# Performance work log

Measured on AMD Instinct MI355X. Metric: run time of the kernel, lower is better.

The kernel has to match this reference:

```python
import jax, jax.numpy as jnp
from jax import lax
import numpy as np

PROB = 0.4
SNR_LO, SNR_HI = 0.5, 3.0
BF_LO, BF_HI = 0.1, 0.5
MAX_CH = 0.5
FS = 256
B, C, T = 64, 64, 15360


def setup_inputs() -> dict:
    key = jax.random.key(0)
    ks = jax.random.split(key, 8)
    return {
        "x": jax.random.normal(ks[0], (B, C, T), dtype=jnp.float32),
        "noise": jax.random.normal(ks[1], (B, C, T), dtype=jnp.float32),
        "apply_u": jax.random.uniform(ks[2], (B,), dtype=jnp.float32),
        "frac_u": jax.random.uniform(ks[3], (B,), dtype=jnp.float32),
        "ch_u": jax.random.uniform(ks[4], (B, C), dtype=jnp.float32),
        "burst_u": jax.random.uniform(ks[5], (B,), dtype=jnp.float32),
        "start_u": jax.random.uniform(ks[6], (B,), dtype=jnp.float32),
        "snr_u": jax.random.uniform(ks[7], (B,), dtype=jnp.float32),
    }


def _emg_inject(x, noise, apply_u, frac_u, ch_u, burst_u, start_u, snr_u):
    b, c, t = x.shape
    # --- highpass: noise - moving average (torch conv1d, zero pad) ---
    k = max(3, FS // 10)
    if k % 2 == 0:
        k += 1  # -> 25
    ker = jnp.ones((1, 1, k), noise.dtype) / k
    low = lax.conv_general_dilated(
        noise.reshape(b * c, 1, t), ker, (1,), [(k // 2, k // 2)],
        dimension_numbers=("NCH", "OIH", "NCH")).reshape(b, c, t)
    emg = noise - low  # (B,C,T)

    # --- per-sample burst mask with linear edge ramps ---
    blen = lax.stop_gradient(jnp.floor(t * (BF_LO + burst_u * (BF_HI - BF_LO))).astype(jnp.int32))  # (B,)
    start = lax.stop_gradient(jnp.floor(start_u * jnp.maximum(t - blen, 1).astype(jnp.float32)).astype(jnp.int32))
    elen = jnp.minimum(25, blen // 4)

    tt = jnp.arange(t, dtype=jnp.float32)[None, :]          # (1,T)
    sf = start.astype(jnp.float32)[:, None]                  # (B,1)
    bf = blen.astype(jnp.float32)[:, None]
    ef = elen.astype(jnp.float32)[:, None]
    end = sf + bf
    denom = jnp.maximum(ef - 1.0, 1.0)
    in_burst = (tt >= sf) & (tt < end)
    up = (tt - sf) / denom                                   # linspace(0,1,elen)
    down = (end - 1.0 - tt) / denom                          # linspace(1,0,elen)
    ramped = jnp.where(tt < sf + ef, up, jnp.where(tt >= end - ef, down, 1.0))
    mask = jnp.where(in_burst, jnp.where(ef > 1.0, ramped, 1.0), 0.0)  # (B,T)

    # --- random affected-channel subset (randperm[:n_affected]) ---
    n_aff = jnp.maximum(1, jnp.floor(c * frac_u * MAX_CH).astype(jnp.int32))  # (B,)
    ch_rank = jnp.argsort(jnp.argsort(ch_u, axis=1), axis=1)                  # (B,C)
    ch_mask = (ch_rank < n_aff[:, None]).astype(x.dtype)                      # (B,C)

    emg_b = emg * mask[:, None, :]
    sig_p = jnp.sqrt(jnp.mean(x * x, axis=-1, keepdims=True)) + 1e-8          # (B,C,1)
    noi_p = jnp.sqrt(jnp.mean(emg_b * emg_b, axis=-1, keepdims=True)) + 1e-8
    snr = (SNR_LO + snr_u * (SNR_HI - SNR_LO))[:, None, None]
    scaled = emg_b * (sig_p / (noi_p * snr))

    sel = (apply_u <= PROB).astype(x.dtype)[:, None, None] * ch_mask[:, :, None]
    return x + sel * scaled


def reference(x, noise, apply_u, frac_u, ch_u, burst_u, start_u, snr_u):
    return _emg_inject(x, noise, apply_u, frac_u, ch_u, burst_u, start_u, snr_u)
```

## Files before the change

### kernel.cpp

```cpp
#include <hip/hip_runtime.h>
#include <math.h>

constexpr int T_LEN = 15360;
constexpr int B_DIM = 64;
constexpr int C_DIM = 64;
constexpr int NTHR  = 256;
constexpr int PT    = T_LEN / NTHR;
constexpr int VPT   = T_LEN / 4 / NTHR;
constexpr int KHALF = 12;

__global__ __launch_bounds__(NTHR, 2)
void emg_inject_kernel(const float* __restrict__ x,
                       const float* __restrict__ noise,
                       const float* __restrict__ apply_u,
                       const float* __restrict__ frac_u,
                       const float* __restrict__ ch_u,
                       const float* __restrict__ burst_u,
                       const float* __restrict__ start_u,
                       const float* __restrict__ snr_u,
                       float* __restrict__ out)
{
    const int row = blockIdx.x;
    const int b   = row >> 6;
    const int c   = row & 63;
    const int tid = threadIdx.x;

    __shared__ float s_ch[C_DIM];
    __shared__ float s_red[8];
    __shared__ float s_noise[T_LEN];

    if (tid < C_DIM) s_ch[tid] = ch_u[(size_t)b * C_DIM + tid];
    __syncthreads();

    const float myv = s_ch[c];
    int rank = 0;
    #pragma unroll 8
    for (int i = 0; i < C_DIM; ++i) {
        float v = s_ch[i];
        rank += (v < myv || (v == myv && i < c)) ? 1 : 0;
    }
    const float frac = frac_u[b];
    int n_aff = (int)floorf(((float)C_DIM * frac) * 0.5f);
    n_aff = max(1, n_aff);
    const bool affected = (apply_u[b] <= 0.4f) && (rank < n_aff);

    const float*  xrow = x   + (size_t)row * T_LEN;
    float*        orow = out + (size_t)row * T_LEN;
    const float4* x4   = (const float4*)xrow;
    float4*       o4   = (float4*)orow;

    if (!affected) {
        #pragma unroll
        for (int it = 0; it < VPT; ++it) {
            int idx = tid + it * NTHR;
            o4[idx] = x4[idx];
        }
        return;
    }

    const float4* n4 = (const float4*)(noise + (size_t)row * T_LEN);
    float4* s_n4 = (float4*)s_noise;
    float4 xr[VPT];
    float sumx2 = 0.f;
    #pragma unroll
    for (int it = 0; it < VPT; ++it) {
        int idx = tid + it * NTHR;
        float4 nv = n4[idx];
        s_n4[idx] = nv;
        float4 xv = x4[idx];
        xr[it] = xv;
        sumx2 += xv.x * xv.x + xv.y * xv.y + xv.z * xv.z + xv.w * xv.w;
    }

    const float bu   = burst_u[b];
    const float bfr  = 0.1f + bu * 0.4f;
    const int   blen = (int)floorf((float)T_LEN * bfr);
    int tmb = T_LEN - blen; if (tmb < 1) tmb = 1;
    const int   start = (int)floorf(start_u[b] * (float)tmb);
    const int   elen  = min(25, blen / 4);
    const float sf    = (float)start;
    const float endf  = sf + (float)blen;
    const float ef    = (float)elen;
    const float denom = fmaxf(ef - 1.0f, 1.0f);
    const float inv_denom = 1.0f / denom;
    const float head_end  = sf + ef;
    const float tail_beg  = endf - ef;

    __syncthreads();

    const int lo = tid * PT;
    float w = 0.f;
    for (int u = lo - KHALF; u <= lo + KHALF; ++u) {
        float v = (u >= 0 && u < T_LEN) ? s_noise[u] : 0.f;
        w += v;
    }
    float e[PT];
    float sume2 = 0.f;
    const float inv_k = 1.0f / 25.0f;
    #pragma unroll
    for (int j = 0; j < PT; ++j) {
        const int t  = lo + j;
        const float nv  = s_noise[t];
        const float emg = nv - w * inv_k;
        const float tt  = (float)t;
        const bool  inb = (tt >= sf) && (tt < endf);
        float ramped;
        if (tt < head_end)       ramped = (tt - sf) * inv_denom;
        else if (tt >= tail_beg) ramped = (endf - 1.0f - tt) * inv_denom;
        else                     ramped = 1.0f;
        const float m  = inb ? ((ef > 1.0f) ? ramped : 1.0f) : 0.0f;
        const float eb = emg * m;
        e[j] = eb;
        sume2 += eb * eb;
        const int ai = t + KHALF + 1;
        const int si = t - KHALF;
        const float av = (ai < T_LEN) ? s_noise[ai] : 0.f;
        const float sv = (si >= 0)    ? s_noise[si] : 0.f;
        w += av - sv;
    }

    __syncthreads();

    #pragma unroll
    for (int j = 0; j < PT; j += 4) {
        float4 v = make_float4(e[j], e[j + 1], e[j + 2], e[j + 3]);
        *(float4*)&s_noise[lo + j] = v;
    }

    float v1 = sumx2, v2 = sume2;
    #pragma unroll
    for (int off = 32; off > 0; off >>= 1) {
        v1 += __shfl_down(v1, off, 64);
        v2 += __shfl_down(v2, off, 64);
    }
    const int wave = tid >> 6;
    if ((tid & 63) == 0) { s_red[wave] = v1; s_red[wave + 4] = v2; }
    __syncthreads();
    const float sx = s_red[0] + s_red[1] + s_red[2] + s_red[3];
    const float se = s_red[4] + s_red[5] + s_red[6] + s_red[7];

    const float sig_p = sqrtf(sx / (float)T_LEN) + 1e-8f;
    const float noi_p = sqrtf(se / (float)T_LEN) + 1e-8f;
    const float snr   = 0.5f + snr_u[b] * 2.5f;
    const float coef  = sig_p / (noi_p * snr);

    #pragma unroll
    for (int it = 0; it < VPT; ++it) {
        int idx = tid + it * NTHR;
        float4 ev = s_n4[idx];
        float4 xv = xr[it];
        float4 ov;
        ov.x = xv.x + coef * ev.x;
        ov.y = xv.y + coef * ev.y;
        ov.z = xv.z + coef * ev.z;
        ov.w = xv.w + coef * ev.w;
        o4[idx] = ov;
    }
}

extern "C" void kernel_launch(void* const* d_in, const int* in_sizes, int n_in,
                              void* d_out, int out_size, void* d_ws, size_t ws_size,
                              hipStream_t stream) {
    const float* x       = (const float*)d_in[0];
    const float* noise   = (const float*)d_in[1];
    const float* apply_u = (const float*)d_in[2];
    const float* frac_u  = (const float*)d_in[3];
    const float* ch_u    = (const float*)d_in[4];
    const float* burst_u = (const float*)d_in[5];
    const float* start_u = (const float*)d_in[6];
    const float* snr_u   = (const float*)d_in[7];
    float* out = (float*)d_out;

    dim3 grid(B_DIM * C_DIM);
    dim3 block(NTHR);
    emg_inject_kernel<<<grid, block, 0, stream>>>(
        x, noise, apply_u, frac_u, ch_u, burst_u, start_u, snr_u, out);
}
```

Before: 143.6 us.

## Stream noise in shared-memory chunks and recompute emg to raise occupancy

Replaces the full-row 60KB shared noise buffer and per-thread register cache of x with a 12KB chunked shared buffer holding halos. Affected rows make two passes over the noise: one to accumulate the emg power and one to recompute the emg and write the output, re-reading x from global memory. This lowers shared memory and register use so more blocks fit per CU (launch bounds raised to 6). In exchange, affected rows read noise twice and x twice and add more barriers.

Result: slower. 282.9 us (+97.1%).

```diff
diff --git a/kernel.cpp b/kernel.cpp
--- a/kernel.cpp
+++ b/kernel.cpp
@@ -5,11 +5,14 @@
 constexpr int B_DIM = 64;
 constexpr int C_DIM = 64;
 constexpr int NTHR  = 256;
-constexpr int PT    = T_LEN / NTHR;
 constexpr int VPT   = T_LEN / 4 / NTHR;
 constexpr int KHALF = 12;
-
-__global__ __launch_bounds__(NTHR, 2)
+constexpr int CH     = 3072;
+constexpr int NCHUNK = T_LEN / CH;
+constexpr int EPT    = CH / NTHR;
+constexpr int F4PT   = CH / 4 / NTHR;
+
+__global__ __launch_bounds__(NTHR, 6)
 void emg_inject_kernel(const float* __restrict__ x,
                        const float* __restrict__ noise,
                        const float* __restrict__ apply_u,
@@ -27,7 +30,7 @@
 
     __shared__ float s_ch[C_DIM];
     __shared__ float s_red[8];
-    __shared__ float s_noise[T_LEN];
+    __shared__ __align__(16) float s_buf[CH + 2 * KHALF + 1];
 
     if (tid < C_DIM) s_ch[tid] = ch_u[(size_t)b * C_DIM + tid];
     __syncthreads();
@@ -45,6 +48,7 @@
     const bool affected = (apply_u[b] <= 0.4f) && (rank < n_aff);
 
     const float*  xrow = x   + (size_t)row * T_LEN;
+    const float*  nrow = noise + (size_t)row * T_LEN;
     float*        orow = out + (size_t)row * T_LEN;
     const float4* x4   = (const float4*)xrow;
     float4*       o4   = (float4*)orow;
@@ -56,20 +60,6 @@
             o4[idx] = x4[idx];
         }
         return;
-    }
-
-    const float4* n4 = (const float4*)(noise + (size_t)row * T_LEN);
-    float4* s_n4 = (float4*)s_noise;
-    float4 xr[VPT];
-    float sumx2 = 0.f;
-    #pragma unroll
-    for (int it = 0; it < VPT; ++it) {
-        int idx = tid + it * NTHR;
-        float4 nv = n4[idx];
-        s_n4[idx] = nv;
-        float4 xv = x4[idx];
-        xr[it] = xv;
-        sumx2 += xv.x * xv.x + xv.y * xv.y + xv.z * xv.z + xv.w * xv.w;
     }
 
     const float bu   = burst_u[b];
@@ -85,46 +75,54 @@
     const float inv_denom = 1.0f / denom;
     const float head_end  = sf + ef;
     const float tail_beg  = endf - ef;
-
-    __syncthreads();
-
-    const int lo = tid * PT;
-    float w = 0.f;
-    for (int u = lo - KHALF; u <= lo + KHALF; ++u) {
-        float v = (u >= 0 && u < T_LEN) ? s_noise[u] : 0.f;
-        w += v;
-    }
-    float e[PT];
+    const float inv_k = 1.0f / 25.0f;
+
+    float sumx2 = 0.f;
+    #pragma unroll
+    for (int it = 0; it < VPT; ++it) {
+        float4 xv = x4[tid + it * NTHR];
+        sumx2 += xv.x * xv.x + xv.y * xv.y + xv.z * xv.z + xv.w * xv.w;
+    }
+
     float sume2 = 0.f;
-    const float inv_k = 1.0f / 25.0f;
-    #pragma unroll
-    for (int j = 0; j < PT; ++j) {
-        const int t  = lo + j;
-        const float nv  = s_noise[t];
-        const float emg = nv - w * inv_k;
-        const float tt  = (float)t;
-        const bool  inb = (tt >= sf) && (tt < endf);
-        float ramped;
-        if (tt < head_end)       ramped = (tt - sf) * inv_denom;
-        else if (tt >= tail_beg) ramped = (endf - 1.0f - tt) * inv_denom;
-        else                     ramped = 1.0f;
-        const float m  = inb ? ((ef > 1.0f) ? ramped : 1.0f) : 0.0f;
-        const float eb = emg * m;
-        e[j] = eb;
-        sume2 += eb * eb;
-        const int ai = t + KHALF + 1;
-        const int si = t - KHALF;
-        const float av = (ai < T_LEN) ? s_noise[ai] : 0.f;
-        const float sv = (si >= 0)    ? s_noise[si] : 0.f;
-        w += av - sv;
-    }
-
-    __syncthreads();
-
-    #pragma unroll
-    for (int j = 0; j < PT; j += 4) {
-        float4 v = make_float4(e[j], e[j + 1], e[j + 2], e[j + 3]);
-        *(float4*)&s_noise[lo + j] = v;
+    for (int ck = 0; ck < NCHUNK; ++ck) {
+        const int g0 = ck * CH;
+        const float4* nsrc = (const float4*)(nrow + g0);
+        float4* sb4 = (float4*)(s_buf + KHALF);
+        #pragma unroll
+        for (int it = 0; it < F4PT; ++it) {
+            int q = tid + it * NTHR;
+            sb4[q] = nsrc[q];
+        }
+        if (tid < KHALF) {
+            int gl = g0 - KHALF + tid;
+            s_buf[tid] = (gl >= 0) ? nrow[gl] : 0.f;
+            int gr = g0 + CH + tid;
+            s_buf[KHALF + CH + tid] = (gr < T_LEN) ? nrow[gr] : 0.f;
+        }
+        __syncthreads();
+
+        const int l0 = KHALF + tid * EPT;
+        float w = 0.f;
+        #pragma unroll
+        for (int d = -KHALF; d <= KHALF; ++d) w += s_buf[l0 + d];
+        #pragma unroll
+        for (int j = 0; j < EPT; ++j) {
+            const float nv  = s_buf[l0 + j];
+            const float emg = nv - w * inv_k;
+            const float tt  = (float)(g0 + tid * EPT + j);
+            const bool  inb = (tt >= sf) && (tt < endf);
+            float ramped;
+            if (tt < head_end)       ramped = (tt - sf) * inv_denom;
+            else if (tt >= tail_beg) ramped = (endf - 1.0f - tt) * inv_denom;
+            else                     ramped = 1.0f;
+            const float m  = inb ? ((ef > 1.0f) ? ramped : 1.0f) : 0.0f;
+            const float eb = emg * m;
+            sume2 += eb * eb;
+            if (j < EPT - 1)
+                w += s_buf[l0 + j + KHALF + 1] - s_buf[l0 + j - KHALF];
+        }
+        __syncthreads();
     }
 
     float v1 = sumx2, v2 = sume2;
@@ -144,17 +142,64 @@
     const float snr   = 0.5f + snr_u[b] * 2.5f;
     const float coef  = sig_p / (noi_p * snr);
 
-    #pragma unroll
-    for (int it = 0; it < VPT; ++it) {
-        int idx = tid + it * NTHR;
-        float4 ev = s_n4[idx];
-        float4 xv = xr[it];
-        float4 ov;
-        ov.x = xv.x + coef * ev.x;
-        ov.y = xv.y + coef * ev.y;
-        ov.z = xv.z + coef * ev.z;
-        ov.w = xv.w + coef * ev.w;
-        o4[idx] = ov;
+    for (int ck = 0; ck < NCHUNK; ++ck) {
+        const int g0 = ck * CH;
+        const float4* nsrc = (const float4*)(nrow + g0);
+        float4* sb4 = (float4*)(s_buf + KHALF);
+        #pragma unroll
+        for (int it = 0; it < F4PT; ++it) {
+            int q = tid + it * NTHR;
+            sb4[q] = nsrc[q];
+        }
+        if (tid < KHALF) {
+            int gl = g0 - KHALF + tid;
+            s_buf[tid] = (gl >= 0) ? nrow[gl] : 0.f;
+            int gr = g0 + CH + tid;
+            s_buf[KHALF + CH + tid] = (gr < T_LEN) ? nrow[gr] : 0.f;
+        }
+        __syncthreads();
+
+        const int l0 = KHALF + tid * EPT;
+        float w = 0.f;
+        #pragma unroll
+        for (int d = -KHALF; d <= KHALF; ++d) w += s_buf[l0 + d];
+        float e[EPT];
+        #pragma unroll
+        for (int j = 0; j < EPT; ++j) {
+            const float nv  = s_buf[l0 + j];
+            const float emg = nv - w * inv_k;
+            const float tt  = (float)(g0 + tid * EPT + j);
+            const bool  inb = (tt >= sf) && (tt < endf);
+            float ramped;
+            if (tt < head_end)       ramped = (tt - sf) * inv_denom;
+            else if (tt >= tail_beg) ramped = (endf - 1.0f - tt) * inv_denom;
+            else                     ramped = 1.0f;
+            const float m  = inb ? ((ef > 1.0f) ? ramped : 1.0f) : 0.0f;
+            e[j] = emg * m;
+            if (j < EPT - 1)
+                w += s_buf[l0 + j + KHALF + 1] - s_buf[l0 + j - KHALF];
+        }
+        __syncthreads();
+
+        #pragma unroll
+        for (int j = 0; j < EPT; ++j) s_buf[l0 + j] = e[j];
+        __syncthreads();
+
+        const float4* xsrc = (const float4*)(xrow + g0);
+        float4*       odst = (float4*)(orow + g0);
+        #pragma unroll
+        for (int it = 0; it < F4PT; ++it) {
+            int q = tid + it * NTHR;
+            float4 ev = sb4[q];
+            float4 xv = xsrc[q];
+            float4 ov;
+            ov.x = xv.x + coef * ev.x;
+            ov.y = xv.y + coef * ev.y;
+            ov.z = xv.z + coef * ev.z;
+            ov.w = xv.w + coef * ev.w;
+            odst[q] = ov;
+        }
+        __syncthreads();
     }
 }
 
```
